# Performance work log

Hardware: AMD Instinct MI355X
Metric: run time of the kernel (lower is better)

Reference implementation:

```python
import jax, jax.numpy as jnp
import numpy as np

B, L, F = 16, 1024, 64
D = 256          # d_model (expand_factor=1 -> d_inner == d_model)
S = 2            # num_scales
N = 16           # state_size
H = 32           # fc hidden
EPS = 1e-5


def setup_inputs() -> dict:
    key = jax.random.key(0)
    ks = jax.random.split(key, 20)
    g = lambda i, shape, s=0.05: jax.random.normal(ks[i], shape, dtype=jnp.float32) * s
    return {
        "x": jax.random.normal(ks[0], (B, L, F), dtype=jnp.float32),
        "W_in": g(1, (F, D)), "b_in": jnp.zeros((D,), jnp.float32),
        # per-scale liquid-Mamba params, stacked over scales
        "Wd": g(2, (S, D, D)), "bd": jnp.zeros((S, D), jnp.float32),
        "WB": g(3, (S, D, N)), "WC": g(4, (S, D, N)),
        "Wtau": g(5, (S, D, D)),
        "A_log": jnp.broadcast_to(jnp.log(jnp.arange(1, N + 1, dtype=jnp.float32)), (S, D, N)).copy(),
        "Dp": jnp.ones((S, D), jnp.float32),
        "Wout": g(6, (S, D, D)),
        # head
        "ln_g": jnp.ones((D,), jnp.float32), "ln_b": jnp.zeros((D,), jnp.float32),
        "W1": g(7, (D, H)), "b1": jnp.zeros((H,), jnp.float32),
        "W2": g(8, (H, 1)), "b2": jnp.zeros((1,), jnp.float32),
    }


def _liquid_ssm(x, Wd, bd, WB, WC, Wtau, A_log, Dp, Wout):
    # x: [B,L,D] -> y: [B,L,D]. Selective scan with liquid time-constant gate.
    delta = jax.nn.softplus(jnp.einsum('bld,de->ble', x, Wd) + bd)   # [B,L,D]
    tau = jax.nn.sigmoid(jnp.einsum('bld,de->ble', x, Wtau))          # liquid gate
    delta = delta * tau
    Bm = jnp.einsum('bld,dn->bln', x, WB)                             # [B,L,N]
    Cm = jnp.einsum('bld,dn->bln', x, WC)                             # [B,L,N]
    A = -jnp.exp(A_log)                                               # [D,N]
    dA = jnp.exp(delta[..., None] * A)                                # [B,L,D,N]
    dBx = delta[..., None] * Bm[:, :, None, :] * x[..., None]         # [B,L,D,N]

    def step(h, inp):
        a_t, bx_t, c_t = inp                                          # [B,D,N],[B,D,N],[B,N]
        h = a_t * h + bx_t
        y = jnp.einsum('bdn,bn->bd', h, c_t)
        return h, y

    h0 = jnp.zeros((x.shape[0], x.shape[2], A.shape[1]), x.dtype)
    _, ys = jax.lax.scan(step, h0,
                         (dA.transpose(1, 0, 2, 3), dBx.transpose(1, 0, 2, 3), Cm.transpose(1, 0, 2)))
    y = ys.transpose(1, 0, 2) + x * Dp                                # skip connection
    return jnp.einsum('bld,de->ble', y, Wout)


def reference(x, W_in, b_in, Wd, bd, WB, WC, Wtau, A_log, Dp, Wout,
              ln_g, ln_b, W1, b1, W2, b2):
    h = jnp.einsum('blf,fd->bld', x, W_in) + b_in                     # input projection
    outs = [_liquid_ssm(h, Wd[s], bd[s], WB[s], WC[s], Wtau[s], A_log[s], Dp[s], Wout[s])
            for s in range(Wd.shape[0])]
    mamba_out = sum(outs) / len(outs)                                 # average over scales
    last = mamba_out[:, -1, :]                                        # [B,D]
    mu = jnp.mean(last, axis=-1, keepdims=True)
    var = jnp.var(last, axis=-1, keepdims=True)
    z = (last - mu) * jax.lax.rsqrt(var + EPS) * ln_g + ln_b          # LayerNorm
    z = jax.nn.relu(z @ W1 + b1)                                      # dropout is identity in eval
    return z @ W2 + b2                                                # [B,1]
```

## Files before the change

### kernel.cpp

```cpp
#include <hip/hip_runtime.h>
#include <hip/hip_bf16.h>
#include <math.h>

#define B_   16
#define L_   1024
#define F_   64
#define D_   256
#define S_   2
#define N_   16
#define H_   32
#define EPS_ 1e-5f
#define BL_  (B_*L_)
#define NCH_ 8
#define TC_  (L_/NCH_)
#define SUB_ 64
#define TSTR_ 68
#define LOG2E_ 1.44269504088896340736f
#define XBLK_ (BL_*F_/1024)

typedef __attribute__((ext_vector_type(8))) short  bf16x8;
typedef __attribute__((ext_vector_type(4))) float  f32x4;
typedef __attribute__((ext_vector_type(2))) float  f32x2;

typedef const __attribute__((address_space(1))) void* gas_ptr;
typedef __attribute__((address_space(3))) void*       las_ptr;

#if defined(__has_builtin)
# if __has_builtin(__builtin_amdgcn_exp2f)
#  define EXP2(x) __builtin_amdgcn_exp2f(x)
#  define ASCALE_ LOG2E_
# endif
#endif
#ifndef EXP2
# define EXP2(x) __expf(x)
# define ASCALE_ 1.0f
#endif

__device__ inline void async_copy16(const void* g, void* l) {
    __builtin_amdgcn_global_load_lds((gas_ptr)g, (las_ptr)l, 16, 0, 0);
}

__device__ inline unsigned short f2bf_rne(float x) {
    union { float f; unsigned u; } v; v.f = x;
    unsigned r = v.u + 0x7fff + ((v.u >> 16) & 1);
    return (unsigned short)(r >> 16);
}
__device__ inline float bf2f(unsigned short h) {
    union { float f; unsigned u; } v; v.u = ((unsigned)h) << 16;
    return v.f;
}

__global__ __launch_bounds__(256) void k_prep(const float* __restrict__ x,
                                              const float* __restrict__ Win,
                                              const float* __restrict__ bin,
                                              const float* __restrict__ Wd,
                                              const float* __restrict__ bd,
                                              const float* __restrict__ Wt,
                                              const float* __restrict__ WB,
                                              unsigned short* __restrict__ x_hi,
                                              unsigned short* __restrict__ x_lo,
                                              unsigned short* __restrict__ Weff_hi,
                                              unsigned short* __restrict__ Weff_lo,
                                              float* __restrict__ bias_eff,
                                              unsigned short* __restrict__ WinT_hi,
                                              unsigned short* __restrict__ WinT_lo,
                                              unsigned short* __restrict__ WBe_hi,
                                              unsigned short* __restrict__ WBe_lo,
                                              float* __restrict__ bbias)
{
    const int blk = blockIdx.x;
    const int tid = threadIdx.x;

    if (blk < XBLK_) {
        const int i = (blk * 256 + tid) * 4;
        float4 v = *(const float4*)(x + i);
        ushort4 h4, l4;
        unsigned short hh;
        hh = f2bf_rne(v.x); h4.x = hh; l4.x = f2bf_rne(v.x - bf2f(hh));
        hh = f2bf_rne(v.y); h4.y = hh; l4.y = f2bf_rne(v.y - bf2f(hh));
        hh = f2bf_rne(v.z); h4.z = hh; l4.z = f2bf_rne(v.z - bf2f(hh));
        hh = f2bf_rne(v.w); h4.w = hh; l4.w = f2bf_rne(v.w - bf2f(hh));
        *(ushort4*)(x_hi + i) = h4;
        *(ushort4*)(x_lo + i) = l4;
        return;
    }

    const int job4 = blk - XBLK_;
    const int j    = tid >> 6;
    const int f    = tid & 63;
    const int job  = job4 * 4 + j;

    __shared__ float col[4][D_];

    if (job < 1024) {
        const int s = job >> 9, n = job & 511;
        const float* W = (n < 256) ? (Wd + (size_t)s * D_ * D_) : (Wt + (size_t)s * D_ * D_);
        const int e = n & 255;
        for (int d = f; d < D_; d += 64) col[j][d] = W[(size_t)d * D_ + e];
        __syncthreads();
        float a = 0.f;
        for (int d = 0; d < D_; ++d) a += Win[(size_t)f * D_ + d] * col[j][d];
        unsigned short hi = f2bf_rne(a);
        size_t o = ((size_t)s * 512 + n) * F_ + f;
        Weff_hi[o] = hi;
        Weff_lo[o] = f2bf_rne(a - bf2f(hi));
        if (f == 0) {
            float bb = 0.f;
            for (int d = 0; d < D_; ++d) bb += bin[d] * col[j][d];
            if (n < 256) bb += bd[s * D_ + e];
            bias_eff[s * 512 + n] = bb;
        }
    } else if (job < 1024 + D_) {
        const int d = job - 1024;
        float v = Win[(size_t)f * D_ + d];
        unsigned short hi = f2bf_rne(v);
        size_t o = (size_t)d * F_ + f;
        WinT_hi[o] = hi;
        WinT_lo[o] = f2bf_rne(v - bf2f(hi));
    } else {
        const int idx = job - (1024 + D_);
        const int s = idx >> 4, n = idx & 15;
        const float* wb = WB + (size_t)s * D_ * N_;
        float a = 0.f;
        for (int d = 0; d < D_; ++d) a += Win[(size_t)f * D_ + d] * wb[(size_t)d * N_ + n];
        unsigned short hi = f2bf_rne(a);
        size_t o = ((size_t)s * N_ + n) * F_ + f;
        WBe_hi[o] = hi;
        WBe_lo[o] = f2bf_rne(a - bf2f(hi));
        if (f == 0) {
            float bb = 0.f;
            for (int d = 0; d < D_; ++d) bb += bin[d] * wb[(size_t)d * N_ + n];
            bbias[s * N_ + n] = bb;
        }
    }
}

__global__ __launch_bounds__(256) void k_fused_scan(
        const unsigned short* __restrict__ x_hi,
        const unsigned short* __restrict__ x_lo,
        const unsigned short* __restrict__ Weff_hi,
        const unsigned short* __restrict__ Weff_lo,
        const unsigned short* __restrict__ WinT_hi,
        const unsigned short* __restrict__ WinT_lo,
        const unsigned short* __restrict__ WBe_hi,
        const unsigned short* __restrict__ WBe_lo,
        const float* __restrict__ bias_eff,
        const float* __restrict__ bin,
        const float* __restrict__ bbias,
        const float* __restrict__ A_log,
        float* __restrict__ part,
        float* __restrict__ csum)
{
    const int dtile = blockIdx.x >> 3;
    const int c     = blockIdx.x & 7;
    const int b     = blockIdx.y;
    const int s     = blockIdx.z;
    const int d0    = dtile * 16;
    const int tid   = threadIdx.x;
    const int wid   = tid >> 6;
    const int lane  = tid & 63;
    const int l15   = lane & 15;
    const int quad  = lane >> 4;
    const int dl    = tid & 15;
    const int nl    = tid >> 4;

    __shared__ unsigned short Wh[64 * F_];
    __shared__ unsigned short Wl[64 * F_];
    __shared__ float sdl[16][TSTR_];
    __shared__ float sq [16][TSTR_];
    __shared__ float sb [16][TSTR_];

    const int r8 = lane >> 3;
    const int c8 = lane & 7;

    #pragma unroll
    for (int call = 0; call < 2; ++call) {
        const int rr = call * 8 + r8;
        const int ar = wid * 16 + rr;
        const int lc = (c8 - ar) & 7;
        const unsigned short *gh, *gl;
        if (wid == 0)      { size_t o = ((size_t)s * 512 + d0 + rr) * F_ + lc * 8;       gh = Weff_hi + o; gl = Weff_lo + o; }
        else if (wid == 1) { size_t o = ((size_t)s * 512 + 256 + d0 + rr) * F_ + lc * 8; gh = Weff_hi + o; gl = Weff_lo + o; }
        else if (wid == 2) { size_t o = ((size_t)(d0 + rr)) * F_ + lc * 8;               gh = WinT_hi + o; gl = WinT_lo + o; }
        else               { size_t o = ((size_t)s * N_ + rr) * F_ + lc * 8;             gh = WBe_hi + o;  gl = WBe_lo + o; }
        async_copy16(gh, &Wh[(wid * 16 + call * 8) * F_]);
        async_copy16(gl, &Wl[(wid * 16 + call * 8) * F_]);
    }

    const float bias_d = bias_eff[s * 512 + d0 + l15];
    const float bias_t = bias_eff[s * 512 + 256 + d0 + l15];
    const float bin_v  = bin[d0 + l15];
    const float bb_v   = bbias[s * N_ + l15];
    const float A2 = -__expf(A_log[((size_t)s * D_ + d0 + dl) * N_ + nl]) * ASCALE_;

    f32x2 st01 = {0.f, 0.f};
    f32x2 st23 = {0.f, 0.f};
    float As = 0.f;

    const int qoff = quad * 8;
    const int nsc  = TC_ / SUB_;

    bf16x8 fah0, fah1, fal0, fal1;
    {
        const size_t rowb = ((size_t)b * L_ + c * TC_ + (nsc - 1) * SUB_ + wid * 16 + l15) * F_;
        fah0 = *(const bf16x8*)(x_hi + rowb + qoff);
        fah1 = *(const bf16x8*)(x_hi + rowb + 32 + qoff);
        fal0 = *(const bf16x8*)(x_lo + rowb + qoff);
        fal1 = *(const bf16x8*)(x_lo + rowb + 32 + qoff);
    }
    __syncthreads();

    for (int sc = nsc - 1; sc >= 0; --sc) {
        f32x4 acc[4];
        #pragma unroll
        for (int g = 0; g < 4; ++g) acc[g] = (f32x4){0.f, 0.f, 0.f, 0.f};
        #pragma unroll
        for (int ks = 0; ks < 2; ++ks) {
            bf16x8 ah = ks ? fah1 : fah0;
            bf16x8 al = ks ? fal1 : fal0;
            #pragma unroll
            for (int g = 0; g < 4; ++g) {
                const int brow = g * 16 + l15;
                const int pcB  = ((ks * 4 + quad) + brow) & 7;
                bf16x8 bh = *(const bf16x8*)&Wh[brow * F_ + pcB * 8];
                bf16x8 bl = *(const bf16x8*)&Wl[brow * F_ + pcB * 8];
                acc[g] = __builtin_amdgcn_mfma_f32_16x16x32_bf16(ah, bh, acc[g], 0, 0, 0);
                acc[g] = __builtin_amdgcn_mfma_f32_16x16x32_bf16(ah, bl, acc[g], 0, 0, 0);
                acc[g] = __builtin_amdgcn_mfma_f32_16x16x32_bf16(al, bh, acc[g], 0, 0, 0);
            }
        }

        bf16x8 nah0, nah1, nal0, nal1;
        const bool more = (sc > 0);
        if (more) {
            const size_t rowb = ((size_t)b * L_ + c * TC_ + (sc - 1) * SUB_ + wid * 16 + l15) * F_;
            nah0 = *(const bf16x8*)(x_hi + rowb + qoff);
            nah1 = *(const bf16x8*)(x_hi + rowb + 32 + qoff);
            nal0 = *(const bf16x8*)(x_lo + rowb + qoff);
            nal1 = *(const bf16x8*)(x_lo + rowb + 32 + qoff);
        }

        __syncthreads();

        {
            f32x4 wd_, wq_, wb_;
            #pragma unroll
            for (int r = 0; r < 4; ++r) {
                const float pd  = acc[0][r] + bias_d;
                const float sp  = fmaxf(pd, 0.f) + __logf(1.f + __expf(-fabsf(pd)));
                const float sg  = 1.f / (1.f + __expf(-(acc[1][r] + bias_t)));
                const float dlt = sp * sg;
                const float hv  = acc[2][r] + bin_v;
                wd_[r] = dlt;
                wq_[r] = dlt * hv;
                wb_[r] = acc[3][r] + bb_v;
            }
            const int tcol = wid * 16 + quad * 4;
            *(f32x4*)&sdl[l15][tcol] = wd_;
            *(f32x4*)&sq [l15][tcol] = wq_;
            *(f32x4*)&sb [l15][tcol] = wb_;
        }
        __syncthreads();

        #pragma unroll 4
        for (int tt = SUB_ - 4; tt >= 0; tt -= 4) {
            f32x4 dp = *(const f32x4*)&sdl[dl][tt];
            f32x4 qp = *(const f32x4*)&sq [dl][tt];
            f32x4 bp = *(const f32x4*)&sb [nl][tt];
            const float a2v = fmaf(A2, dp.w, As);
            const float a1v = fmaf(A2, dp.z, a2v);
            const float a0v = fmaf(A2, dp.y, a1v);
            f32x2 e01, e23;
            e23.y = EXP2(As);
            e23.x = EXP2(a2v);
            e01.y = EXP2(a1v);
            e01.x = EXP2(a0v);
            f32x2 q01 = {qp.x, qp.y}, q23 = {qp.z, qp.w};
            f32x2 b01 = {bp.x, bp.y}, b23 = {bp.z, bp.w};
            st01 = q01 * b01 * e01 + st01;
            st23 = q23 * b23 * e23 + st23;
            As = fmaf(A2, dp.x, a0v);
        }

        if (more) { fah0 = nah0; fah1 = nah1; fal0 = nal0; fal1 = nal1; }
    }

    const size_t pb = ((size_t)s * B_ + b) * NCH_ + c;
    part[(pb * D_ + d0 + dl) * N_ + nl] = (st01.x + st01.y) + (st23.x + st23.y);
    if (nl == 0)
        csum[pb * D_ + d0 + dl] = As / A2;
}

__global__ __launch_bounds__(256) void k_final(const float* __restrict__ x,
                                               const float* __restrict__ Win,
                                               const float* __restrict__ bin,
                                               const float* __restrict__ part,
                                               const float* __restrict__ csum,
                                               const float* __restrict__ A_log,
                                               const float* __restrict__ WC,
                                               const float* __restrict__ Dp,
                                               const float* __restrict__ Wout,
                                               const float* __restrict__ ln_g,
                                               const float* __restrict__ ln_b,
                                               const float* __restrict__ W1,
                                               const float* __restrict__ b1,
                                               const float* __restrict__ W2,
                                               const float* __restrict__ b2,
                                               float* __restrict__ out)
{
    const int b   = blockIdx.x;
    const int tid = threadIdx.x;

    __shared__ float xr[F_];
    __shared__ float hl[D_];
    __shared__ float cm[S_][N_];
    __shared__ float ys[S_][D_];
    __shared__ float zv[D_];
    __shared__ float red1[256];
    __shared__ float red2[256];
    __shared__ float r1[H_];

    if (tid < F_) xr[tid] = x[((size_t)b * L_ + (L_ - 1)) * F_ + tid];
    __syncthreads();

    {
        float a = bin[tid];
        for (int f = 0; f < F_; ++f) a += xr[f] * Win[(size_t)f * D_ + tid];
        hl[tid] = a;
    }
    __syncthreads();

    if (tid < S_ * N_) {
        int s = tid >> 4, n = tid & 15;
        float a = 0.f;
        for (int d = 0; d < D_; ++d) a += hl[d] * WC[((size_t)s * D_ + d) * N_ + n];
        cm[s][n] = a;
    }
    __syncthreads();

    for (int s = 0; s < S_; ++s) {
        const float* al = A_log + ((size_t)s * D_ + tid) * N_;
        float a2v[N_];
        #pragma unroll
        for (int n = 0; n < N_; ++n) a2v[n] = -__expf(al[n]);
        const size_t cbase = ((size_t)s * B_ + b) * NCH_;
        float cs[NCH_];
        #pragma unroll
        for (int c = 0; c < NCH_; ++c) cs[c] = csum[(cbase + c) * D_ + tid];
        float acc = 0.f;
        float tail = 0.f;
        #pragma unroll
        for (int c = NCH_ - 1; c >= 0; --c) {
            const float* pp = part + ((cbase + c) * D_ + tid) * N_;
            #pragma unroll
            for (int n = 0; n < N_; ++n)
                acc += cm[s][n] * __expf(a2v[n] * tail) * pp[n];
            tail += cs[c];
        }
        ys[s][tid] = acc + hl[tid] * Dp[s * D_ + tid];
    }
    __syncthreads();

    float v;
    {
        float a = 0.f;
        for (int s = 0; s < S_; ++s) {
            const float* wo = Wout + (size_t)s * D_ * D_;
            for (int d = 0; d < D_; ++d) a += ys[s][d] * wo[(size_t)d * D_ + tid];
        }
        v = a * (1.f / S_);
    }

    red1[tid] = v;
    red2[tid] = v * v;
    __syncthreads();
    for (int off = 128; off > 0; off >>= 1) {
        if (tid < off) { red1[tid] += red1[tid + off]; red2[tid] += red2[tid + off]; }
        __syncthreads();
    }
    const float mu  = red1[0] * (1.f / D_);
    const float var = red2[0] * (1.f / D_) - mu * mu;
    const float z = (v - mu) * rsqrtf(var + EPS_) * ln_g[tid] + ln_b[tid];
    zv[tid] = z;
    __syncthreads();

    if (tid < H_) {
        float a = b1[tid];
        for (int e = 0; e < D_; ++e) a += zv[e] * W1[(size_t)e * H_ + tid];
        r1[tid] = fmaxf(a, 0.f);
    }
    __syncthreads();
    if (tid == 0) {
        float a = b2[0];
        for (int j = 0; j < H_; ++j) a += r1[j] * W2[j];
        out[b] = a;
    }
}

extern "C" void kernel_launch(void* const* d_in, const int* in_sizes, int n_in,
                              void* d_out, int out_size, void* d_ws, size_t ws_size,
                              hipStream_t stream)
{
    const float* x     = (const float*)d_in[0];
    const float* Win   = (const float*)d_in[1];
    const float* bin   = (const float*)d_in[2];
    const float* Wd    = (const float*)d_in[3];
    const float* bd    = (const float*)d_in[4];
    const float* WB    = (const float*)d_in[5];
    const float* WC    = (const float*)d_in[6];
    const float* Wtau  = (const float*)d_in[7];
    const float* A_log = (const float*)d_in[8];
    const float* Dp    = (const float*)d_in[9];
    const float* Wout  = (const float*)d_in[10];
    const float* ln_g  = (const float*)d_in[11];
    const float* ln_b  = (const float*)d_in[12];
    const float* W1    = (const float*)d_in[13];
    const float* b1    = (const float*)d_in[14];
    const float* W2    = (const float*)d_in[15];
    const float* b2    = (const float*)d_in[16];
    float* out = (float*)d_out;

    char* ws = (char*)d_ws;
    const size_t MB = 1024 * 1024;
    const size_t KB = 1024;
    unsigned short* x_hi     = (unsigned short*)(ws);
    unsigned short* x_lo     = (unsigned short*)(ws + 2 * MB);
    unsigned short* Weff_hi  = (unsigned short*)(ws + 4 * MB);
    unsigned short* Weff_lo  = (unsigned short*)(ws + 4 * MB + 128 * KB);
    unsigned short* WinT_hi  = (unsigned short*)(ws + 4 * MB + 256 * KB);
    unsigned short* WinT_lo  = (unsigned short*)(ws + 4 * MB + 288 * KB);
    unsigned short* WBe_hi   = (unsigned short*)(ws + 4 * MB + 320 * KB);
    unsigned short* WBe_lo   = (unsigned short*)(ws + 4 * MB + 324 * KB);
    float*          bias_eff = (float*)(ws + 4 * MB + 328 * KB);
    float*          bbias    = (float*)(ws + 4 * MB + 332 * KB);
    float*          part     = (float*)(ws + 5 * MB);
    float*          csum     = (float*)(ws + 9 * MB);

    hipLaunchKernelGGL(k_prep, dim3(XBLK_ + 328), dim3(256), 0, stream,
                       x, Win, bin, Wd, bd, Wtau, WB,
                       x_hi, x_lo, Weff_hi, Weff_lo, bias_eff,
                       WinT_hi, WinT_lo, WBe_hi, WBe_lo, bbias);
    hipLaunchKernelGGL(k_fused_scan, dim3((D_ / 16) * NCH_, B_, S_), dim3(256), 0, stream,
                       x_hi, x_lo, Weff_hi, Weff_lo, WinT_hi, WinT_lo, WBe_hi, WBe_lo,
                       bias_eff, bin, bbias, A_log, part, csum);
    hipLaunchKernelGGL(k_final, dim3(B_), dim3(256), 0, stream,
                       x, Win, bin, part, csum, A_log, WC, Dp, Wout,
                       ln_g, ln_b, W1, b1, W2, b2, out);
}
```

Baseline: 187.9 us.

## Split final tail kernel into three kernels to raise block-level parallelism

The single 16-block final kernel becomes three launches. One does the chunk combine per (scale, batch) using 32 blocks, and the WC projection is spread across all threads. The next does the Wout projection over 64 blocks with a split-K reduction. The last runs only LayerNorm and the MLP head. The goal is to spread the serial tail over more CUs, at the cost of two extra launches and round trips through global memory.

```diff
diff --git a/kernel.cpp b/kernel.cpp
--- a/kernel.cpp
+++ b/kernel.cpp
@@ -291,86 +291,120 @@
         csum[pb * D_ + d0 + dl] = As / A2;
 }
 
-__global__ __launch_bounds__(256) void k_final(const float* __restrict__ x,
-                                               const float* __restrict__ Win,
-                                               const float* __restrict__ bin,
-                                               const float* __restrict__ part,
-                                               const float* __restrict__ csum,
-                                               const float* __restrict__ A_log,
-                                               const float* __restrict__ WC,
-                                               const float* __restrict__ Dp,
-                                               const float* __restrict__ Wout,
-                                               const float* __restrict__ ln_g,
-                                               const float* __restrict__ ln_b,
-                                               const float* __restrict__ W1,
-                                               const float* __restrict__ b1,
-                                               const float* __restrict__ W2,
-                                               const float* __restrict__ b2,
-                                               float* __restrict__ out)
+__global__ __launch_bounds__(256) void k_ys(const float* __restrict__ x,
+                                            const float* __restrict__ Win,
+                                            const float* __restrict__ bin,
+                                            const float* __restrict__ part,
+                                            const float* __restrict__ csum,
+                                            const float* __restrict__ A_log,
+                                            const float* __restrict__ WC,
+                                            const float* __restrict__ Dp,
+                                            float* __restrict__ ys)
+{
+    const int s   = blockIdx.x;
+    const int b   = blockIdx.y;
+    const int tid = threadIdx.x;
+
+    __shared__ float xr[F_];
+    __shared__ float hl[D_];
+    __shared__ float cm[N_];
+    __shared__ float cred[N_][17];
+
+    if (tid < F_) xr[tid] = x[((size_t)b * L_ + (L_ - 1)) * F_ + tid];
+    __syncthreads();
+
+    {
+        float a = bin[tid];
+        for (int f = 0; f < F_; ++f) a += xr[f] * Win[(size_t)f * D_ + tid];
+        hl[tid] = a;
+    }
+    __syncthreads();
+
+    {
+        const int n  = tid & 15;
+        const int dq = tid >> 4;
+        float a = 0.f;
+        for (int d = dq * 16; d < dq * 16 + 16; ++d)
+            a += hl[d] * WC[((size_t)s * D_ + d) * N_ + n];
+        cred[n][dq] = a;
+    }
+    __syncthreads();
+    if (tid < N_) {
+        float a = 0.f;
+        #pragma unroll
+        for (int q = 0; q < 16; ++q) a += cred[tid][q];
+        cm[tid] = a;
+    }
+    __syncthreads();
+
+    const float* al = A_log + ((size_t)s * D_ + tid) * N_;
+    float a2v[N_];
+    #pragma unroll
+    for (int n = 0; n < N_; ++n) a2v[n] = -__expf(al[n]);
+    const size_t cbase = ((size_t)s * B_ + b) * NCH_;
+    float acc = 0.f;
+    float tail = 0.f;
+    for (int c = NCH_ - 1; c >= 0; --c) {
+        const float* pp = part + ((cbase + c) * D_ + tid) * N_;
+        #pragma unroll
+        for (int n = 0; n < N_; ++n)
+            acc += cm[n] * __expf(a2v[n] * tail) * pp[n];
+        tail += csum[(cbase + c) * D_ + tid];
+    }
+    ys[((size_t)s * B_ + b) * D_ + tid] = acc + hl[tid] * Dp[s * D_ + tid];
+}
+
+__global__ __launch_bounds__(256) void k_last(const float* __restrict__ ys,
+                                              const float* __restrict__ Wout,
+                                              float* __restrict__ last)
+{
+    const int b  = blockIdx.x;
+    const int e0 = blockIdx.y * 64;
+    const int tid = threadIdx.x;
+    const int e  = tid & 63;
+    const int kq = tid >> 6;
+
+    __shared__ float ysl[S_ * D_];
+    __shared__ float red[4][64];
+
+    #pragma unroll
+    for (int j = tid; j < S_ * D_; j += 256) {
+        const int ss = j >> 8, dd = j & 255;
+        ysl[j] = ys[((size_t)ss * B_ + b) * D_ + dd];
+    }
+    __syncthreads();
+
+    float a = 0.f;
+    for (int k = kq * 128; k < kq * 128 + 128; ++k) {
+        const int ss = k >> 8, dd = k & 255;
+        a += ysl[k] * Wout[((size_t)ss * D_ + dd) * D_ + e0 + e];
+    }
+    red[kq][e] = a;
+    __syncthreads();
+    if (kq == 0) {
+        const float v = (red[0][e] + red[1][e] + red[2][e] + red[3][e]) * (1.f / S_);
+        last[(size_t)b * D_ + e0 + e] = v;
+    }
+}
+
+__global__ __launch_bounds__(256) void k_head(const float* __restrict__ last,
+                                              const float* __restrict__ ln_g,
+                                              const float* __restrict__ ln_b,
+                                              const float* __restrict__ W1,
+                                              const float* __restrict__ b1,
+                                              const float* __restrict__ W2,
+                                              const float* __restrict__ b2,
+                                              float* __restrict__ out)
 {
     const int b   = blockIdx.x;
     const int tid = threadIdx.x;
 
-    __shared__ float xr[F_];
-    __shared__ float hl[D_];
-    __shared__ float cm[S_][N_];
-    __shared__ float ys[S_][D_];
     __shared__ float zv[D_];
     __shared__ float red1[256];
     __shared__ float red2[256];
     __shared__ float r1[H_];
 
-    if (tid < F_) xr[tid] = x[((size_t)b * L_ + (L_ - 1)) * F_ + tid];
-    __syncthreads();
-
-    {
-        float a = bin[tid];
-        for (int f = 0; f < F_; ++f) a += xr[f] * Win[(size_t)f * D_ + tid];
-        hl[tid] = a;
-    }
-    __syncthreads();
-
-    if (tid < S_ * N_) {
-        int s = tid >> 4, n = tid & 15;
-        float a = 0.f;
-        for (int d = 0; d < D_; ++d) a += hl[d] * WC[((size_t)s * D_ + d) * N_ + n];
-        cm[s][n] = a;
-    }
-    __syncthreads();
-
-    for (int s = 0; s < S_; ++s) {
-        const float* al = A_log + ((size_t)s * D_ + tid) * N_;
-        float a2v[N_];
-        #pragma unroll
-        for (int n = 0; n < N_; ++n) a2v[n] = -__expf(al[n]);
-        const size_t cbase = ((size_t)s * B_ + b) * NCH_;
-        float cs[NCH_];
-        #pragma unroll
-        for (int c = 0; c < NCH_; ++c) cs[c] = csum[(cbase + c) * D_ + tid];
-        float acc = 0.f;
-        float tail = 0.f;
-        #pragma unroll
-        for (int c = NCH_ - 1; c >= 0; --c) {
-            const float* pp = part + ((cbase + c) * D_ + tid) * N_;
-            #pragma unroll
-            for (int n = 0; n < N_; ++n)
-                acc += cm[s][n] * __expf(a2v[n] * tail) * pp[n];
-            tail += cs[c];
-        }
-        ys[s][tid] = acc + hl[tid] * Dp[s * D_ + tid];
-    }
-    __syncthreads();
-
-    float v;
-    {
-        float a = 0.f;
-        for (int s = 0; s < S_; ++s) {
-            const float* wo = Wout + (size_t)s * D_ * D_;
-            for (int d = 0; d < D_; ++d) a += ys[s][d] * wo[(size_t)d * D_ + tid];
-        }
-        v = a * (1.f / S_);
-    }
-
+    const float v = last[(size_t)b * D_ + tid];
     red1[tid] = v;
     red2[tid] = v * v;
     __syncthreads();
@@ -435,6 +469,8 @@
     float*          bbias    = (float*)(ws + 4 * MB + 332 * KB);
     float*          part     = (float*)(ws + 5 * MB);
     float*          csum     = (float*)(ws + 9 * MB);
+    float*          ysbuf    = (float*)(ws + 9 * MB + 256 * KB);
+    float*          lastbuf  = (float*)(ws + 9 * MB + 512 * KB);
 
     hipLaunchKernelGGL(k_prep, dim3(XBLK_ + 328), dim3(256), 0, stream,
                        x, Win, bin, Wd, bd, Wtau, WB,
@@ -443,7 +479,9 @@
     hipLaunchKernelGGL(k_fused_scan, dim3((D_ / 16) * NCH_, B_, S_), dim3(256), 0, stream,
                        x_hi, x_lo, Weff_hi, Weff_lo, WinT_hi, WinT_lo, WBe_hi, WBe_lo,
                        bias_eff, bin, bbias, A_log, part, csum);
-    hipLaunchKernelGGL(k_final, dim3(B_), dim3(256), 0, stream,
-                       x, Win, bin, part, csum, A_log, WC, Dp, Wout,
-                       ln_g, ln_b, W1, b1, W2, b2, out);
-}
+    hipLaunchKernelGGL(k_ys,   dim3(S_, B_), dim3(256), 0, stream,
+                       x, Win, bin, part, csum, A_log, WC, Dp, ysbuf);
+    hipLaunchKernelGGL(k_last, dim3(B_, 4), dim3(256), 0, stream, ysbuf, Wout, lastbuf);
+    hipLaunchKernelGGL(k_head, dim3(B_), dim3(256), 0, stream,
+                       lastbuf, ln_g, ln_b, W1, b1, W2, b2, out);
+}
```

After: 164.7 us. 1.14x faster.
